# Kernel optimization log

Measured on AMD Instinct MI355X. Metric: run time of the kernel, lower is better.

The kernel has to match this reference:

```python
import jax, jax.numpy as jnp
import numpy as np


def setup_inputs() -> dict:
    key = jax.random.key(0)
    k1, k2, k3 = jax.random.split(key, 3)
    B, N, D = 16, 4096, 64
    q = jax.random.normal(k1, (B, N, D), dtype=jnp.float32)
    k = jax.random.normal(k2, (B, N, D), dtype=jnp.float32)
    v = jax.random.normal(k3, (B, N, D), dtype=jnp.float32)
    return {"q": q, "k": k, "v": v}


def reference(q, k, v):
    # attention = softmax(q @ k^T, axis=2)  (scale=None in the torch module,
    # dropout=0.0 is identity)
    scores = jnp.einsum("bnd,bmd->bnm", q, k)          # [B, N, N]
    attention = jax.nn.softmax(scores, axis=2)          # softmax over keys
    context = jnp.einsum("bnm,bmd->bnd", attention, v)  # [B, N, D]
    return (context, attention)
```

## Files before the change

### kernel.cpp

```cpp
#include <hip/hip_runtime.h>
#include <hip/hip_bf16.h>

typedef _Float16 half8 __attribute__((ext_vector_type(8)));
typedef _Float16 half4 __attribute__((ext_vector_type(4)));
typedef short short8 __attribute__((ext_vector_type(8)));
typedef short short4v __attribute__((ext_vector_type(4)));
typedef float f32x4 __attribute__((ext_vector_type(4)));

#define BATCH 16
#define SEQ   4096
#define DIM   64
#define KVB   64
#define NCH   (SEQ / KVB)
#define NSC   (NCH / 2)
#define EL_CH 4096
#define EL_B  (NCH * EL_CH)

__device__ __forceinline__ short f2bf(float f) {
    unsigned u = __builtin_bit_cast(unsigned, f);
    u += 0x7FFF + ((u >> 16) & 1);
    return (short)(u >> 16);
}
__device__ __forceinline__ float bf2f(short h) {
    return __builtin_bit_cast(float, (unsigned)((unsigned short)h) << 16);
}

__device__ __forceinline__ void gld16(const void* g, void* l) {
    __builtin_amdgcn_global_load_lds(
        (const __attribute__((address_space(1))) unsigned int*)g,
        (__attribute__((address_space(3))) unsigned int*)l, 16, 0, 0);
}

__global__ __launch_bounds__(256) void preconvert(
    const float* __restrict__ k, const float* __restrict__ v,
    _Float16* __restrict__ kh, _Float16* __restrict__ vh)
{
    int f = blockIdx.x * 256 + threadIdx.x;
    int lane = f & 63;
    int sub  = (f >> 6) & 7;
    int ch   = (f >> 9) & 63;
    int bb   = (f >> 15) & 15;
    int isV  = f >> 19;
    int nf = sub >> 1, kk = sub & 1;
    size_t fo = (size_t)(f & ((1 << 19) - 1)) * 8;

    if (!isV) {
        int key = ch * 64 + nf * 16 + (lane & 15);
        int d0  = kk * 32 + (lane >> 4) * 8;
        const float* src = k + (((size_t)bb * SEQ + key) * DIM + d0);
        half8 h8;
        #pragma unroll
        for (int e = 0; e < 8; ++e) h8[e] = (_Float16)src[e];
        *(half8*)(kh + fo) = h8;
    } else {
        int kr0 = kk * 32 + (lane >> 4) * 8;
        int d   = nf * 16 + (lane & 15);
        const float* src = v + (((size_t)bb * SEQ + ch * 64 + kr0) * DIM + d);
        half8 h8;
        #pragma unroll
        for (int e = 0; e < 8; ++e) h8[e] = (_Float16)src[e * DIM];
        *(half8*)(vh + fo) = h8;
    }
}

__global__ __launch_bounds__(512, 4) void attn_main(
    const float* __restrict__ q, const _Float16* __restrict__ kh,
    const _Float16* __restrict__ vh, float* __restrict__ ctx,
    float* __restrict__ att)
{
    __shared__ _Float16 KV[2][8192];
    __shared__ _Float16 Ph[8][16][72];

    int id = blockIdx.x;
    int bb = (id & 7) + 8 * (id >> 8);
    int qt = (id >> 3) & 31;

    int tid = threadIdx.x;
    int w = tid >> 6, lane = tid & 63, li = lane & 15, h4 = lane >> 4;

    int qrow = qt * 128 + w * 16 + li;
    const float* qp = q + ((size_t)bb * SEQ + qrow) * DIM;
    half8 aq[2];
    #pragma unroll
    for (int kk = 0; kk < 2; ++kk)
        #pragma unroll
        for (int e = 0; e < 8; ++e)
            aq[kk][e] = (_Float16)qp[kk * 32 + h4 * 8 + e];

    const _Float16* khb = kh + (size_t)bb * EL_B;
    const _Float16* vvb = vh + (size_t)bb * EL_B;

    auto qkt = [&](const _Float16* base, f32x4* s) {
        const half8* k8 = (const half8*)base;
        #pragma unroll
        for (int kk = 0; kk < 2; ++kk)
            #pragma unroll
            for (int nf = 0; nf < 4; ++nf)
                s[nf] = __builtin_amdgcn_mfma_f32_16x16x32_f16(
                    k8[(nf * 2 + kk) * 64 + lane], aq[kk], s[nf], 0, 0, 0);
    };

    float ll = 0.f;

    auto stage_sc = [&](int buf, int sc) {
        const _Float16* g = khb + (size_t)sc * (2 * EL_CH) + tid * 8;
        gld16(g,        &KV[buf][w * 512]);
        gld16(g + 4096, &KV[buf][4096 + w * 512]);
    };

    stage_sc(0, 0);
    for (int sc = 0; sc < NSC; ++sc) {
        int buf = sc & 1;
        if (sc + 1 < NSC) {
            stage_sc(buf ^ 1, sc + 1);
            asm volatile("s_waitcnt vmcnt(2)" ::: "memory");
        } else {
            asm volatile("s_waitcnt vmcnt(0)" ::: "memory");
        }
        __builtin_amdgcn_s_barrier();
        asm volatile("" ::: "memory");

        #pragma unroll
        for (int c2 = 0; c2 < 2; ++c2) {
            f32x4 s[4];
            #pragma unroll
            for (int nf = 0; nf < 4; ++nf) s[nf] = (f32x4){0.f, 0.f, 0.f, 0.f};
            qkt(&KV[buf][c2 * EL_CH], s);
            float a = 0.f;
            #pragma unroll
            for (int nf = 0; nf < 4; ++nf)
                #pragma unroll
                for (int r = 0; r < 4; ++r)
                    a += __expf(s[nf][r]);
            ll += a;
        }

        asm volatile("" ::: "memory");
        __builtin_amdgcn_s_barrier();
    }

    ll += __shfl_xor(ll, 16);
    ll += __shfl_xor(ll, 32);
    float rl = 1.0f / ll;

    f32x4 acc[4];
    #pragma unroll
    for (int nf = 0; nf < 4; ++nf) acc[nf] = (f32x4){0.f, 0.f, 0.f, 0.f};

    float* attb = att + ((size_t)bb * SEQ + (size_t)qt * 128 + w * 16) * SEQ;

    auto stage_k = [&](int buf, int ch) {
        const _Float16* g = khb + (size_t)ch * EL_CH + tid * 8;
        gld16(g, &KV[0][buf * EL_CH + w * 512]);
    };
    auto stage_v = [&](int buf, int ch) {
        const _Float16* g = vvb + (size_t)ch * EL_CH + tid * 8;
        gld16(g, &KV[1][buf * EL_CH + w * 512]);
    };

    stage_k(0, 0); stage_v(0, 0);
    for (int ch = 0; ch < NCH; ++ch) {
        int buf = ch & 1;
        if (ch + 1 < NCH) {
            stage_k(buf ^ 1, ch + 1);
            stage_v(buf ^ 1, ch + 1);
            if (ch == 0) asm volatile("s_waitcnt vmcnt(2)" ::: "memory");
            else         asm volatile("s_waitcnt vmcnt(6)" ::: "memory");
        } else {
            asm volatile("s_waitcnt vmcnt(4)" ::: "memory");
        }
        __builtin_amdgcn_s_barrier();
        asm volatile("" ::: "memory");

        f32x4 s[4];
        #pragma unroll
        for (int nf = 0; nf < 4; ++nf) s[nf] = (f32x4){0.f, 0.f, 0.f, 0.f};
        qkt(&KV[0][buf * EL_CH], s);

        #pragma unroll
        for (int nf = 0; nf < 4; ++nf) {
            half4 p4;
            #pragma unroll
            for (int r = 0; r < 4; ++r)
                p4[r] = (_Float16)(__expf(s[nf][r]) * rl);
            *(half4*)&Ph[w][li][nf * 16 + h4 * 4] = p4;
        }

        #pragma unroll
        for (int j = 0; j < 4; ++j) {
            int row = j * 4 + h4;
            half4 ph = *(const half4*)&Ph[w][row][li * 4];
            f32x4 pv = { (float)ph[0], (float)ph[1], (float)ph[2], (float)ph[3] };
            __builtin_nontemporal_store(
                pv, (f32x4*)(attb + (size_t)row * SEQ + ch * KVB + li * 4));
        }

        const half8* v8 = (const half8*)&KV[1][buf * EL_CH];
        #pragma unroll
        for (int kk = 0; kk < 2; ++kk) {
            half8 pa = *(const half8*)&Ph[w][li][kk * 32 + h4 * 8];
            #pragma unroll
            for (int nf = 0; nf < 4; ++nf)
                acc[nf] = __builtin_amdgcn_mfma_f32_16x16x32_f16(
                    pa, v8[(nf * 2 + kk) * 64 + lane], acc[nf], 0, 0, 0);
        }

        asm volatile("" ::: "memory");
        __builtin_amdgcn_s_barrier();
    }

    float* ctxb = ctx + ((size_t)bb * SEQ + (size_t)qt * 128 + w * 16) * DIM;
    #pragma unroll
    for (int nf = 0; nf < 4; ++nf)
        #pragma unroll
        for (int r = 0; r < 4; ++r)
            __builtin_nontemporal_store(
                acc[nf][r], &ctxb[(size_t)(4 * h4 + r) * DIM + nf * 16 + li]);
}

__global__ __launch_bounds__(256) void attn_fallback(
    const float* __restrict__ q, const float* __restrict__ k,
    const float* __restrict__ v, float* __restrict__ ctx,
    float* __restrict__ att)
{
    __shared__ short K_hi[KVB][72];
    __shared__ short K_lo[KVB][72];
    __shared__ short V_lds[DIM][72];
    __shared__ short P_lds[4][16][72];

    int id = blockIdx.x;
    int bb = (id & 7) + 8 * (id >> 9);
    int qt = (id >> 3) & 63;
    int tid = threadIdx.x;
    int w = tid >> 6, lane = tid & 63, li = lane & 15, h4 = lane >> 4;

    int qrow = qt * 64 + w * 16 + li;
    const float* qp = q + ((size_t)bb * SEQ + qrow) * DIM;
    short8 aq[2], aql[2];
    #pragma unroll
    for (int kk = 0; kk < 2; ++kk)
        #pragma unroll
        for (int e = 0; e < 8; ++e) {
            float x = qp[kk * 32 + h4 * 8 + e];
            short h = f2bf(x);
            aq[kk][e] = h; aql[kk][e] = f2bf(x - bf2f(h));
        }

    float m[4], l[4];
    #pragma unroll
    for (int r = 0; r < 4; ++r) { m[r] = -3.0e38f; l[r] = 0.0f; }
    const float* kbase = k + (size_t)bb * SEQ * DIM;
    const float* vbase = v + (size_t)bb * SEQ * DIM;

    for (int ch = 0; ch < NCH; ++ch) {
        __syncthreads();
        const float4* kc = (const float4*)(kbase + (size_t)ch * KVB * DIM);
        #pragma unroll
        for (int j = 0; j < 4; ++j) {
            int f4 = j * 256 + tid; int key = f4 >> 4, d4 = f4 & 15;
            float4 val = kc[f4];
            short4v h4v, l4v;
            h4v[0]=f2bf(val.x); l4v[0]=f2bf(val.x-bf2f(h4v[0]));
            h4v[1]=f2bf(val.y); l4v[1]=f2bf(val.y-bf2f(h4v[1]));
            h4v[2]=f2bf(val.z); l4v[2]=f2bf(val.z-bf2f(h4v[2]));
            h4v[3]=f2bf(val.w); l4v[3]=f2bf(val.w-bf2f(h4v[3]));
            *(short4v*)&K_hi[key][d4*4] = h4v;
            *(short4v*)&K_lo[key][d4*4] = l4v;
        }
        __syncthreads();
        f32x4 s[4];
        #pragma unroll
        for (int nf = 0; nf < 4; ++nf) s[nf] = (f32x4){0.f,0.f,0.f,0.f};
        #pragma unroll
        for (int kk = 0; kk < 2; ++kk)
            #pragma unroll
            for (int nf = 0; nf < 4; ++nf) {
                short8 kbv = *(const short8*)&K_hi[nf*16+li][kk*32+h4*8];
                short8 klv = *(const short8*)&K_lo[nf*16+li][kk*32+h4*8];
                s[nf] = __builtin_amdgcn_mfma_f32_16x16x32_bf16(aq[kk],  kbv, s[nf],0,0,0);
                s[nf] = __builtin_amdgcn_mfma_f32_16x16x32_bf16(aq[kk],  klv, s[nf],0,0,0);
                s[nf] = __builtin_amdgcn_mfma_f32_16x16x32_bf16(aql[kk], kbv, s[nf],0,0,0);
            }
        #pragma unroll
        for (int r = 0; r < 4; ++r) {
            float cmax = fmaxf(fmaxf(s[0][r],s[1][r]), fmaxf(s[2][r],s[3][r]));
            #pragma unroll
            for (int off = 1; off < 16; off <<= 1) cmax = fmaxf(cmax, __shfl_xor(cmax, off));
            float mnew = fmaxf(m[r], cmax);
            float cs = __expf(s[0][r]-mnew)+__expf(s[1][r]-mnew)+__expf(s[2][r]-mnew)+__expf(s[3][r]-mnew);
            #pragma unroll
            for (int off = 1; off < 16; off <<= 1) cs += __shfl_xor(cs, off);
            l[r] = l[r]*__expf(m[r]-mnew) + cs; m[r] = mnew;
        }
    }
    float rl[4];
    #pragma unroll
    for (int r = 0; r < 4; ++r) rl[r] = 1.0f / l[r];

    f32x4 acc[4];
    #pragma unroll
    for (int nf = 0; nf < 4; ++nf) acc[nf] = (f32x4){0.f,0.f,0.f,0.f};
    float* attb = att + ((size_t)bb * SEQ + (size_t)qt * 64 + w * 16) * SEQ;

    for (int ch = 0; ch < NCH; ++ch) {
        __syncthreads();
        const float4* kc = (const float4*)(kbase + (size_t)ch * KVB * DIM);
        #pragma unroll
        for (int j = 0; j < 4; ++j) {
            int f4 = j * 256 + tid; int key = f4 >> 4, d4 = f4 & 15;
            float4 val = kc[f4];
            short4v h4v, l4v;
            h4v[0]=f2bf(val.x); l4v[0]=f2bf(val.x-bf2f(h4v[0]));
            h4v[1]=f2bf(val.y); l4v[1]=f2bf(val.y-bf2f(h4v[1]));
            h4v[2]=f2bf(val.z); l4v[2]=f2bf(val.z-bf2f(h4v[2]));
            h4v[3]=f2bf(val.w); l4v[3]=f2bf(val.w-bf2f(h4v[3]));
            *(short4v*)&K_hi[key][d4*4] = h4v;
            *(short4v*)&K_lo[key][d4*4] = l4v;
        }
        {
            int key = tid & 63, dblk = (tid >> 6) * 16;
            const float* vc = vbase + ((size_t)ch * KVB + key) * DIM + dblk;
            #pragma unroll
            for (int j = 0; j < 4; ++j) {
                float4 val = *(const float4*)(vc + j * 4);
                V_lds[dblk+j*4+0][key]=f2bf(val.x); V_lds[dblk+j*4+1][key]=f2bf(val.y);
                V_lds[dblk+j*4+2][key]=f2bf(val.z); V_lds[dblk+j*4+3][key]=f2bf(val.w);
            }
        }
        __syncthreads();
        f32x4 s[4];
        #pragma unroll
        for (int nf = 0; nf < 4; ++nf) s[nf] = (f32x4){0.f,0.f,0.f,0.f};
        #pragma unroll
        for (int kk = 0; kk < 2; ++kk)
            #pragma unroll
            for (int nf = 0; nf < 4; ++nf) {
                short8 kbv = *(const short8*)&K_hi[nf*16+li][kk*32+h4*8];
                short8 klv = *(const short8*)&K_lo[nf*16+li][kk*32+h4*8];
                s[nf] = __builtin_amdgcn_mfma_f32_16x16x32_bf16(aq[kk],  kbv, s[nf],0,0,0);
                s[nf] = __builtin_amdgcn_mfma_f32_16x16x32_bf16(aq[kk],  klv, s[nf],0,0,0);
                s[nf] = __builtin_amdgcn_mfma_f32_16x16x32_bf16(aql[kk], kbv, s[nf],0,0,0);
            }
        #pragma unroll
        for (int nf = 0; nf < 4; ++nf)
            #pragma unroll
            for (int r = 0; r < 4; ++r) {
                float p = __expf(s[nf][r] - m[r]) * rl[r];
                __builtin_nontemporal_store(p, &attb[(size_t)(4*h4+r)*SEQ + ch*KVB + nf*16 + li]);
                P_lds[w][4*h4+r][nf*16+li] = f2bf(p);
            }
        #pragma unroll
        for (int kk = 0; kk < 2; ++kk) {
            short8 pa = *(const short8*)&P_lds[w][li][kk*32+h4*8];
            #pragma unroll
            for (int nf = 0; nf < 4; ++nf) {
                short8 vbv = *(const short8*)&V_lds[nf*16+li][kk*32+h4*8];
                acc[nf] = __builtin_amdgcn_mfma_f32_16x16x32_bf16(pa, vbv, acc[nf],0,0,0);
            }
        }
    }
    float* ctxb = ctx + ((size_t)bb * SEQ + (size_t)qt * 64 + w * 16) * DIM;
    #pragma unroll
    for (int nf = 0; nf < 4; ++nf)
        #pragma unroll
        for (int r = 0; r < 4; ++r)
            __builtin_nontemporal_store(acc[nf][r], &ctxb[(size_t)(4*h4+r)*DIM + nf*16 + li]);
}

extern "C" void kernel_launch(void* const* d_in, const int* in_sizes, int n_in,
                              void* d_out, int out_size, void* d_ws, size_t ws_size,
                              hipStream_t stream) {
    const float* q = (const float*)d_in[0];
    const float* k = (const float*)d_in[1];
    const float* v = (const float*)d_in[2];
    float* ctx = (float*)d_out;
    float* att = (float*)d_out + (size_t)BATCH * SEQ * DIM;

    const size_t t_el = (size_t)BATCH * EL_B;
    const size_t need = 2 * t_el * 2;

    if (ws_size >= need) {
        _Float16* kh = (_Float16*)d_ws;
        _Float16* vh = kh + t_el;
        preconvert<<<4096, 256, 0, stream>>>(k, v, kh, vh);
        attn_main<<<512, 512, 0, stream>>>(q, kh, vh, ctx, att);
    } else {
        attn_fallback<<<BATCH * (SEQ / 64), 256, 0, stream>>>(q, k, v, ctx, att);
    }
}
```

Measured before the change: 289.8 us.

## Process two KV chunks per iteration in the second attention pass

The second pass now stages 128 keys (two 64-key chunks) of K and V per barrier step instead of 64. That halves the number of barriers and loop iterations, and each iteration writes 128-wide attention row segments. LDS grows to separate double-buffered K and V stages plus a wider P buffer, and launch bounds drop from 4 to 2 blocks per SM. The result is lower occupancy in exchange for larger, less frequently synchronized steps.

```diff
diff --git a/kernel.cpp b/kernel.cpp
--- a/kernel.cpp
+++ b/kernel.cpp
@@ -14,7 +14,9 @@
 #define NCH   (SEQ / KVB)
 #define NSC   (NCH / 2)
 #define EL_CH 4096
+#define EL_SC 8192
 #define EL_B  (NCH * EL_CH)
+#define PHS   136
 
 __device__ __forceinline__ short f2bf(float f) {
     unsigned u = __builtin_bit_cast(unsigned, f);
@@ -63,13 +65,14 @@
     }
 }
 
-__global__ __launch_bounds__(512, 4) void attn_main(
+__global__ __launch_bounds__(512, 2) void attn_main(
     const float* __restrict__ q, const _Float16* __restrict__ kh,
     const _Float16* __restrict__ vh, float* __restrict__ ctx,
     float* __restrict__ att)
 {
-    __shared__ _Float16 KV[2][8192];
-    __shared__ _Float16 Ph[8][16][72];
+    __shared__ __align__(16) _Float16 Kst[2][EL_SC];
+    __shared__ __align__(16) _Float16 Vst[2][EL_SC];
+    __shared__ __align__(16) _Float16 Ph[8][16][PHS];
 
     int id = blockIdx.x;
     int bb = (id & 7) + 8 * (id >> 8);
@@ -103,9 +106,9 @@
     float ll = 0.f;
 
     auto stage_sc = [&](int buf, int sc) {
-        const _Float16* g = khb + (size_t)sc * (2 * EL_CH) + tid * 8;
-        gld16(g,        &KV[buf][w * 512]);
-        gld16(g + 4096, &KV[buf][4096 + w * 512]);
+        const _Float16* g = khb + (size_t)sc * EL_SC + tid * 8;
+        gld16(g,        &Kst[buf][w * 512]);
+        gld16(g + 4096, &Kst[buf][4096 + w * 512]);
     };
 
     stage_sc(0, 0);
@@ -125,7 +128,7 @@
             f32x4 s[4];
             #pragma unroll
             for (int nf = 0; nf < 4; ++nf) s[nf] = (f32x4){0.f, 0.f, 0.f, 0.f};
-            qkt(&KV[buf][c2 * EL_CH], s);
+            qkt(&Kst[buf][c2 * EL_CH], s);
             float a = 0.f;
             #pragma unroll
             for (int nf = 0; nf < 4; ++nf)
@@ -149,60 +152,73 @@
 
     float* attb = att + ((size_t)bb * SEQ + (size_t)qt * 128 + w * 16) * SEQ;
 
-    auto stage_k = [&](int buf, int ch) {
-        const _Float16* g = khb + (size_t)ch * EL_CH + tid * 8;
-        gld16(g, &KV[0][buf * EL_CH + w * 512]);
+    auto stage_k2 = [&](int buf, int sc) {
+        const _Float16* g = khb + (size_t)sc * EL_SC + tid * 8;
+        gld16(g,        &Kst[buf][w * 512]);
+        gld16(g + 4096, &Kst[buf][4096 + w * 512]);
     };
-    auto stage_v = [&](int buf, int ch) {
-        const _Float16* g = vvb + (size_t)ch * EL_CH + tid * 8;
-        gld16(g, &KV[1][buf * EL_CH + w * 512]);
+    auto stage_v2 = [&](int buf, int sc) {
+        const _Float16* g = vvb + (size_t)sc * EL_SC + tid * 8;
+        gld16(g,        &Vst[buf][w * 512]);
+        gld16(g + 4096, &Vst[buf][4096 + w * 512]);
     };
 
-    stage_k(0, 0); stage_v(0, 0);
-    for (int ch = 0; ch < NCH; ++ch) {
-        int buf = ch & 1;
-        if (ch + 1 < NCH) {
-            stage_k(buf ^ 1, ch + 1);
-            stage_v(buf ^ 1, ch + 1);
-            if (ch == 0) asm volatile("s_waitcnt vmcnt(2)" ::: "memory");
-            else         asm volatile("s_waitcnt vmcnt(6)" ::: "memory");
+    stage_k2(0, 0); stage_v2(0, 0);
+    for (int sc = 0; sc < NSC; ++sc) {
+        int buf = sc & 1;
+        if (sc + 1 < NSC) {
+            stage_k2(buf ^ 1, sc + 1);
+            stage_v2(buf ^ 1, sc + 1);
+            if (sc == 0) asm volatile("s_waitcnt vmcnt(4)"  ::: "memory");
+            else         asm volatile("s_waitcnt vmcnt(12)" ::: "memory");
         } else {
-            asm volatile("s_waitcnt vmcnt(4)" ::: "memory");
+            asm volatile("s_waitcnt vmcnt(8)" ::: "memory");
         }
         __builtin_amdgcn_s_barrier();
         asm volatile("" ::: "memory");
 
-        f32x4 s[4];
-        #pragma unroll
-        for (int nf = 0; nf < 4; ++nf) s[nf] = (f32x4){0.f, 0.f, 0.f, 0.f};
-        qkt(&KV[0][buf * EL_CH], s);
-
+        f32x4 sA[4], sB[4];
         #pragma unroll
         for (int nf = 0; nf < 4; ++nf) {
-            half4 p4;
-            #pragma unroll
-            for (int r = 0; r < 4; ++r)
-                p4[r] = (_Float16)(__expf(s[nf][r]) * rl);
-            *(half4*)&Ph[w][li][nf * 16 + h4 * 4] = p4;
+            sA[nf] = (f32x4){0.f, 0.f, 0.f, 0.f};
+            sB[nf] = (f32x4){0.f, 0.f, 0.f, 0.f};
+        }
+        qkt(&Kst[buf][0],     sA);
+        qkt(&Kst[buf][EL_CH], sB);
+
+        #pragma unroll
+        for (int nf = 0; nf < 4; ++nf) {
+            half4 pa, pb;
+            #pragma unroll
+            for (int r = 0; r < 4; ++r) {
+                pa[r] = (_Float16)(__expf(sA[nf][r]) * rl);
+                pb[r] = (_Float16)(__expf(sB[nf][r]) * rl);
+            }
+            *(half4*)&Ph[w][li][nf * 16 + h4 * 4]      = pa;
+            *(half4*)&Ph[w][li][64 + nf * 16 + h4 * 4] = pb;
         }
 
         #pragma unroll
         for (int j = 0; j < 4; ++j) {
             int row = j * 4 + h4;
-            half4 ph = *(const half4*)&Ph[w][row][li * 4];
-            f32x4 pv = { (float)ph[0], (float)ph[1], (float)ph[2], (float)ph[3] };
-            __builtin_nontemporal_store(
-                pv, (f32x4*)(attb + (size_t)row * SEQ + ch * KVB + li * 4));
-        }
-
-        const half8* v8 = (const half8*)&KV[1][buf * EL_CH];
-        #pragma unroll
-        for (int kk = 0; kk < 2; ++kk) {
+            half4 pa = *(const half4*)&Ph[w][row][li * 4];
+            half4 pb = *(const half4*)&Ph[w][row][64 + li * 4];
+            f32x4 va = { (float)pa[0], (float)pa[1], (float)pa[2], (float)pa[3] };
+            f32x4 vb = { (float)pb[0], (float)pb[1], (float)pb[2], (float)pb[3] };
+            float* dst = attb + (size_t)row * SEQ + sc * 128;
+            __builtin_nontemporal_store(va, (f32x4*)(dst + li * 4));
+            __builtin_nontemporal_store(vb, (f32x4*)(dst + 64 + li * 4));
+        }
+
+        const half8* v8 = (const half8*)&Vst[buf][0];
+        #pragma unroll
+        for (int kk = 0; kk < 4; ++kk) {
             half8 pa = *(const half8*)&Ph[w][li][kk * 32 + h4 * 8];
             #pragma unroll
             for (int nf = 0; nf < 4; ++nf)
                 acc[nf] = __builtin_amdgcn_mfma_f32_16x16x32_f16(
-                    pa, v8[(nf * 2 + kk) * 64 + lane], acc[nf], 0, 0, 0);
+                    pa, v8[(kk >> 1) * 512 + (nf * 2 + (kk & 1)) * 64 + lane],
+                    acc[nf], 0, 0, 0);
         }
 
         asm volatile("" ::: "memory");
```

New measurement: 282.1 us. 2.6% less time.
